# Kernel tuning notes

Measured on AMD Instinct MI355X. Metric: run time of the kernel, lower is better.

The kernel has to match this reference:

```python
import jax, jax.numpy as jnp
import numpy as np

N = 80000
E = 1280000
C_IN, HID, C_OUT = 3, 64, 1
DEPTH = 3
KS = [40000, 20000, 10000]  # ceil(0.5 * n) per pooling level
EPS = 1e-5


def gcn_conv(x, W, src, dst, ew, n, fill=2.0):
    # PyG GCNConv with add_self_loops=True; improved => self-loop weight fill=2.0
    h = x @ W                                           # [n, F]
    deg = jax.ops.segment_sum(ew, dst, num_segments=n) + fill
    dinv = jax.lax.rsqrt(deg)
    norm = dinv[src] * ew * dinv[dst]                   # [E]
    agg = jax.ops.segment_sum(norm[:, None] * h[src], dst, num_segments=n)
    return agg + (fill * dinv * dinv)[:, None] * h      # self-loop term


def batchnorm(x, gamma, beta):
    # BatchNorm1d in training mode: biased batch stats over the node dim
    mu = jnp.mean(x, axis=0)
    var = jnp.var(x, axis=0)
    return gamma * (x - mu) * jax.lax.rsqrt(var + EPS) + beta


def gcn_block(x, src, dst, ew, n, W, gamma, beta, fill=2.0):
    return jax.nn.relu(batchnorm(gcn_conv(x, W, src, dst, ew, n, fill), gamma, beta))


def topk_pool(x, src, dst, ew, w, k):
    # TopKPooling with ReLU nonlinearity: score = relu(x.w / ||w||)
    n = x.shape[0]
    score = jax.nn.relu(x @ w / jnp.linalg.norm(w))
    sc, perm = jax.lax.top_k(score, k)
    xk = x[perm] * sc[:, None]
    # filter_adj with fixed edge count: invalid edges get weight 0 (no-op in GCN)
    mapping = jnp.full((n,), -1, dtype=src.dtype).at[perm].set(
        jnp.arange(k, dtype=src.dtype))
    ns, nd = mapping[src], mapping[dst]
    valid = (ns >= 0) & (nd >= 0)
    ns = jnp.where(valid, ns, 0)
    nd = jnp.where(valid, nd, 0)
    new_ew = jnp.where(valid, ew, jnp.zeros((), ew.dtype))
    return xk, ns, nd, new_ew, perm


def _forward(x, edge_index, Wd, gd, bd, pw, Wu, gu, bu, W_out):
    src, dst = edge_index[0], edge_index[1]
    ew = jnp.ones(src.shape, x.dtype)
    n = x.shape[0]
    x = gcn_block(x, src, dst, ew, n, Wd[0], gd[0], bd[0])
    xs, sds, ews, perms = [x], [(src, dst)], [ew], []
    for i in range(DEPTH):
        x, src, dst, ew, perm = topk_pool(x, src, dst, ew, pw[i], KS[i])
        x = gcn_block(x, src, dst, ew, KS[i], Wd[i + 1], gd[i + 1], bd[i + 1])
        if i < DEPTH - 1:
            xs.append(x); sds.append((src, dst)); ews.append(ew)
        perms.append(perm)
    for i in range(DEPTH):
        j = DEPTH - 1 - i
        res = xs[j]; src, dst = sds[j]; ew = ews[j]; perm = perms[j]
        up = jnp.zeros_like(res).at[perm].set(x)
        x = res + up
        if i < DEPTH - 1:
            x = gcn_block(x, src, dst, ew, res.shape[0], Wu[i], gu[i], bu[i])
        else:
            x = jax.nn.sigmoid(
                gcn_conv(x, W_out, src, dst, ew, res.shape[0], fill=1.0))
    return x


def setup_inputs() -> dict:
    key = jax.random.key(0)
    ks = jax.random.split(key, 16)
    nrm = lambda k, shape: jax.random.normal(k, shape, jnp.float32) * 0.1
    inp = {
        "x": jax.random.normal(ks[0], (N, C_IN), jnp.float32),
        "edge_index": jax.random.randint(ks[1], (2, E), 0, N, jnp.int32),
    }
    dims = [(C_IN, HID)] + [(HID, HID)] * DEPTH
    ki = 2
    for l, (a, b) in enumerate(dims):
        inp[f"W_d{l}"] = nrm(ks[ki], (a, b)); ki += 1
        inp[f"g_d{l}"] = jnp.ones((b,), jnp.float32)
        inp[f"b_d{l}"] = jnp.zeros((b,), jnp.float32)
    for l in range(DEPTH):
        inp[f"pw{l}"] = nrm(ks[ki], (HID,)); ki += 1
    for l in range(DEPTH - 1):
        inp[f"W_u{l}"] = nrm(ks[ki], (HID, HID)); ki += 1
        inp[f"g_u{l}"] = jnp.ones((HID,), jnp.float32)
        inp[f"b_u{l}"] = jnp.zeros((HID,), jnp.float32)
    inp["W_out"] = nrm(ks[ki], (HID, C_OUT))
    return inp


def reference(x, edge_index, W_d0, g_d0, b_d0, W_d1, g_d1, b_d1, W_d2, g_d2,
              b_d2, W_d3, g_d3, b_d3, pw0, pw1, pw2, W_u0, g_u0, b_u0,
              W_u1, g_u1, b_u1, W_out):
    Wd = [W_d0, W_d1, W_d2, W_d3]
    gd = [g_d0, g_d1, g_d2, g_d3]
    bd = [b_d0, b_d1, b_d2, b_d3]
    pw = [pw0, pw1, pw2]
    Wu = [W_u0, W_u1]
    gu = [g_u0, g_u1]
    bu = [b_u0, b_u1]
    return _forward(x, edge_index, Wd, gd, bd, pw, Wu, gu, bu, W_out)
```

## Files before the change

kernel.cpp:

```cpp
#include <hip/hip_runtime.h>
#include <cstdint>
#include <utility>

#define NN0 80000
#define NE 1280000
#define MMB_GRID 1024
#define EB 2048
#define ENB 625

static inline int cdiv(int a, int b){ return (a+b-1)/b; }

__global__ void k_matmul_bn(const float* __restrict__ x, const float* __restrict__ W,
                            float* __restrict__ h, float* __restrict__ part, int n){
  __shared__ float ls[64], lq[64];
  int f = threadIdx.x & 63;
  float sa = 0.f, sq = 0.f;
  int total = n*64, stride = gridDim.x*blockDim.x;
  for (int t = blockIdx.x*blockDim.x + threadIdx.x; t < total; t += stride){
    int i = t >> 6;
    const float* xr = x + i*64;
    const float* wc = W + f;
    float s = 0.f;
    #pragma unroll
    for (int k2 = 0; k2 < 64; k2++) s += xr[k2]*wc[k2*64];
    h[t] = s; sa += s; sq += s*s;
  }
  if (threadIdx.x < 64){ ls[threadIdx.x] = 0.f; lq[threadIdx.x] = 0.f; }
  __syncthreads();
  atomicAdd(&ls[f], sa); atomicAdd(&lq[f], sq);
  __syncthreads();
  if (threadIdx.x < 128)
    part[blockIdx.x*128 + threadIdx.x] =
      (threadIdx.x < 64) ? ls[threadIdx.x] : lq[threadIdx.x-64];
}

__global__ void k_matmul_bn3(const float* __restrict__ x, const float* __restrict__ W,
                             float* __restrict__ h, float* __restrict__ part, int n){
  __shared__ float ls[64], lq[64];
  int f = threadIdx.x & 63;
  float sa = 0.f, sq = 0.f;
  int total = n*64, stride = gridDim.x*blockDim.x;
  for (int t = blockIdx.x*blockDim.x + threadIdx.x; t < total; t += stride){
    int i = t >> 6;
    float s = x[i*3]*W[f] + x[i*3+1]*W[64+f] + x[i*3+2]*W[128+f];
    h[t] = s; sa += s; sq += s*s;
  }
  if (threadIdx.x < 64){ ls[threadIdx.x] = 0.f; lq[threadIdx.x] = 0.f; }
  __syncthreads();
  atomicAdd(&ls[f], sa); atomicAdd(&lq[f], sq);
  __syncthreads();
  if (threadIdx.x < 128)
    part[blockIdx.x*128 + threadIdx.x] =
      (threadIdx.x < 64) ? ls[threadIdx.x] : lq[threadIdx.x-64];
}

__global__ void k_stats_reduce(const float* __restrict__ part, float* __restrict__ stats){
  int c = blockIdx.x, lane = threadIdx.x;
  float s = 0.f;
  for (int b = lane; b < MMB_GRID; b += 64) s += part[b*128 + c];
  for (int o = 32; o > 0; o >>= 1) s += __shfl_xor(s, o);
  if (lane == 0) stats[c] = s;
}

__global__ void k_matvec(const float* __restrict__ x, const float* __restrict__ W,
                         float* __restrict__ h1, int n){
  int lane = threadIdx.x & 63, w = threadIdx.x >> 6;
  int wid = blockIdx.x*4 + w, nw = gridDim.x*4;
  float wv = W[lane];
  for (int i = wid; i < n; i += nw){
    float v = x[i*64+lane]*wv;
    for (int o = 32; o > 0; o >>= 1) v += __shfl_xor(v, o);
    if (lane == 0) h1[i] = v;
  }
}

__global__ void k_ehist6(const int* __restrict__ key, int* __restrict__ hist, int shift){
  __shared__ int lh[64];
  if (threadIdx.x < 64) lh[threadIdx.x] = 0;
  __syncthreads();
  int base = blockIdx.x*EB + threadIdx.x;
  #pragma unroll
  for (int u = 0; u < 8; u++)
    atomicAdd(&lh[(key[base + u*256] >> shift) & 63], 1);
  __syncthreads();
  if (threadIdx.x < 64) hist[threadIdx.x*ENB + blockIdx.x] = lh[threadIdx.x];
}

__global__ void k_escatter6(const int* __restrict__ keyin, const int* __restrict__ valin,
                            int* __restrict__ keyout, int* __restrict__ valout,
                            const int* __restrict__ hist, int shift){
  __shared__ int dbase[64], run[64], wcnt[4][64];
  int t = threadIdx.x, lane = t & 63, w = t >> 6;
  if (t < 64){ dbase[t] = hist[t*ENB + blockIdx.x]; run[t] = 0; }
  __syncthreads();
  for (int u = 0; u < 8; u++){
    if (t < 64){ wcnt[0][t]=0; wcnt[1][t]=0; wcnt[2][t]=0; wcnt[3][t]=0; }
    __syncthreads();
    int g = blockIdx.x*EB + u*256 + t;
    int kk = keyin[g], vv = valin[g];
    int d = (kk >> shift) & 63;
    unsigned long long m = ~0ull;
    #pragma unroll
    for (int b = 0; b < 6; b++){
      unsigned long long bal = __ballot((d >> b) & 1);
      m &= ((d >> b) & 1) ? bal : ~bal;
    }
    int rnk = __popcll(m & ((1ull << lane) - 1ull));
    if (rnk == 0) wcnt[w][d] = __popcll(m);
    __syncthreads();
    int off2 = run[d] + rnk;
    for (int w2 = 0; w2 < w; w2++) off2 += wcnt[w2][d];
    int pos = dbase[d] + off2;
    keyout[pos] = kk; valout[pos] = vv;
    __syncthreads();
    if (t < 64) run[t] += wcnt[0][t] + wcnt[1][t] + wcnt[2][t] + wcnt[3][t];
    __syncthreads();
  }
}

__global__ void k_rp_search(const int* __restrict__ skey, int* __restrict__ rp,
                            float* __restrict__ dinvA, float* __restrict__ dinvB, int n){
  int i = blockIdx.x*blockDim.x + threadIdx.x;
  if (i >= n) return;
  int lo = 0, hi = NE;
  while (lo < hi){ int mid = (lo+hi)>>1; if (skey[mid] < i) lo = mid+1; else hi = mid; }
  int a = lo;
  lo = a; hi = NE;
  while (lo < hi){ int mid = (lo+hi)>>1; if (skey[mid] < i+1) lo = mid+1; else hi = mid; }
  int b2 = lo;
  rp[i] = a;
  if (i == n-1) rp[n] = NE;
  float deg = (float)(b2 - a);
  dinvA[i] = 1.0f/sqrtf(deg + 2.f);
  dinvB[i] = 1.0f/sqrtf(deg + 1.f);
}

__global__ void k_scan_part(const int* __restrict__ in, int* __restrict__ bsum, int n){
  __shared__ int ws[256];
  int base = blockIdx.x*1024 + threadIdx.x*4;
  int s = 0;
  #pragma unroll
  for (int u = 0; u < 4; u++){ int i = base+u; if (i < n) s += in[i]; }
  ws[threadIdx.x] = s; __syncthreads();
  for (int st = 128; st > 0; st >>= 1){
    if (threadIdx.x < st) ws[threadIdx.x] += ws[threadIdx.x+st];
    __syncthreads();
  }
  if (threadIdx.x == 0) bsum[blockIdx.x] = ws[0];
}

__global__ void k_scan_fin_rp(const int* __restrict__ in, const int* __restrict__ bsum, int nb,
                              int* __restrict__ rp, float* __restrict__ dinvA, int n){
  __shared__ int bws[256]; __shared__ int ws[256];
  int t = threadIdx.x;
  bws[t] = (t < nb) ? bsum[t] : 0; __syncthreads();
  for (int st = 1; st < 256; st <<= 1){
    int a = (t >= st) ? bws[t-st] : 0; __syncthreads();
    bws[t] += a; __syncthreads();
  }
  int blockoff = (blockIdx.x == 0) ? 0 : bws[blockIdx.x-1];
  int base = blockIdx.x*1024 + t*4;
  int v[4]; int s = 0;
  #pragma unroll
  for (int u = 0; u < 4; u++){ int i = base+u; v[u] = (i < n) ? in[i] : 0; s += v[u]; }
  ws[t] = s; __syncthreads();
  for (int st = 1; st < 256; st <<= 1){
    int a = (t >= st) ? ws[t-st] : 0; __syncthreads();
    ws[t] += a; __syncthreads();
  }
  int off = blockoff + ws[t] - s;
  #pragma unroll
  for (int u = 0; u < 4; u++){
    int i = base+u;
    if (i < n){
      rp[i] = off; off += v[u];
      dinvA[i] = 1.0f/sqrtf((float)v[u] + 2.f);
      if (i == n-1) rp[n] = off;
    }
  }
}

__global__ void k_scan_fin_flat(int* __restrict__ data, const int* __restrict__ bsum, int nb, int n){
  __shared__ int bws[256]; __shared__ int ws[256];
  int t = threadIdx.x;
  bws[t] = (t < nb) ? bsum[t] : 0; __syncthreads();
  for (int st = 1; st < 256; st <<= 1){
    int a = (t >= st) ? bws[t-st] : 0; __syncthreads();
    bws[t] += a; __syncthreads();
  }
  int blockoff = (blockIdx.x == 0) ? 0 : bws[blockIdx.x-1];
  int base = blockIdx.x*1024 + t*4;
  int v[4]; int s = 0;
  #pragma unroll
  for (int u = 0; u < 4; u++){ int i = base+u; v[u] = (i < n) ? data[i] : 0; s += v[u]; }
  ws[t] = s; __syncthreads();
  for (int st = 1; st < 256; st <<= 1){
    int a = (t >= st) ? ws[t-st] : 0; __syncthreads();
    ws[t] += a; __syncthreads();
  }
  int off = blockoff + ws[t] - s;
  #pragma unroll
  for (int u = 0; u < 4; u++){
    int i = base+u;
    if (i < n){ data[i] = off; off += v[u]; }
  }
}

__global__ void k_hist_mapped(const int* __restrict__ rp_p, const int* __restrict__ col_p,
                              const int* __restrict__ mapv, int* __restrict__ indeg, int np){
  int d = blockIdx.x*blockDim.x + threadIdx.x;
  if (d >= np) return;
  int md = mapv[d];
  if (md < 0) return;
  int c = 0, e = rp_p[d+1];
  for (int j = rp_p[d]; j < e; j++) if (mapv[col_p[j]] >= 0) c++;
  indeg[md] = c;
}
__global__ void k_scatter_mapped(const int* __restrict__ rp_p, const int* __restrict__ col_p,
                                 const int* __restrict__ mapv, const int* __restrict__ rp_c,
                                 int* __restrict__ col_c, int np){
  int d = blockIdx.x*blockDim.x + threadIdx.x;
  if (d >= np) return;
  int md = mapv[d];
  if (md < 0) return;
  int pos = rp_c[md], e = rp_p[d+1];
  for (int j = rp_p[d]; j < e; j++){
    int ms = mapv[col_p[j]];
    if (ms >= 0) col_c[pos++] = ms;
  }
}

__global__ void k_gather64(const int* __restrict__ rp, const int* __restrict__ col,
                           const float* __restrict__ dinv, const float* __restrict__ x,
                           float* __restrict__ y, int n){
  int t = blockIdx.x*blockDim.x + threadIdx.x;
  int i = t >> 6, f = t & 63;
  if (i >= n) return;
  int beg = rp[i], end = rp[i+1];
  float di = dinv[i];
  float acc = 0.f;
  for (int j = beg; j < end; j++){
    int s = col[j];
    acc += dinv[s]*x[s*64+f];
  }
  y[i*64+f] = di*acc + 2.f*di*di*x[i*64+f];
}

__global__ void k_gather3(const int* __restrict__ rp, const int* __restrict__ col,
                          const float* __restrict__ dinv, const float* __restrict__ x,
                          float* __restrict__ y, int n){
  int i = blockIdx.x*blockDim.x + threadIdx.x;
  if (i >= n) return;
  int beg = rp[i], end = rp[i+1];
  float di = dinv[i];
  float a0 = 0.f, a1 = 0.f, a2 = 0.f;
  for (int j = beg; j < end; j++){
    int s = col[j];
    float ds = dinv[s];
    a0 += ds*x[s*3+0]; a1 += ds*x[s*3+1]; a2 += ds*x[s*3+2];
  }
  float sl = 2.f*di*di;
  y[i*3+0] = di*a0 + sl*x[i*3+0];
  y[i*3+1] = di*a1 + sl*x[i*3+1];
  y[i*3+2] = di*a2 + sl*x[i*3+2];
}

__global__ void k_gather_sig(const int* __restrict__ rp, const int* __restrict__ col,
                             const float* __restrict__ dinv, const float* __restrict__ h1,
                             float* __restrict__ out, int n){
  int i = blockIdx.x*blockDim.x + threadIdx.x;
  if (i >= n) return;
  int beg = rp[i], end = rp[i+1];
  float di = dinv[i];
  float acc = 0.f;
  for (int j = beg; j < end; j++) acc += dinv[col[j]]*h1[col[j]];
  float v = di*acc + di*di*h1[i];
  out[i] = 1.f/(1.f+expf(-v));
}

__global__ void k_bnrelu(float* __restrict__ x, const float* __restrict__ stats,
                         const float* __restrict__ gamma, const float* __restrict__ beta,
                         int n) {
  int t = blockIdx.x*blockDim.x + threadIdx.x;
  if (t >= n*64) return;
  int f = t & 63;
  float inv_n = 1.0f/(float)n;
  float mu = stats[f]*inv_n;
  float var = stats[64+f]*inv_n - mu*mu;
  float v = gamma[f]*(x[t]-mu)*(1.0f/sqrtf(var+1e-5f)) + beta[f];
  x[t] = fmaxf(v, 0.f);
}

__global__ void k_bnrelu_score(float* __restrict__ x, const float* __restrict__ stats,
                               const float* __restrict__ gamma, const float* __restrict__ beta,
                               const float* __restrict__ pw,
                               float* __restrict__ score, unsigned* __restrict__ key,
                               int* __restrict__ idx, int n, int P){
  int lane = threadIdx.x & 63, w = threadIdx.x >> 6;
  int wid = blockIdx.x*4 + w, nw = gridDim.x*4;
  float inv_n = 1.f/(float)n;
  float mu = stats[lane]*inv_n;
  float var = stats[64+lane]*inv_n - mu*mu;
  float gs = gamma[lane]*(1.f/sqrtf(var+1e-5f));
  float bt = beta[lane];
  float pv = pw[lane];
  float q = pv*pv;
  for (int o = 32; o > 0; o >>= 1) q += __shfl_xor(q, o);
  float qn = 1.f/sqrtf(q);
  for (int i = wid; i < n; i += nw){
    float v = fmaxf(gs*(x[i*64+lane]-mu)+bt, 0.f);
    x[i*64+lane] = v;
    float s = v*pv;
    for (int o = 32; o > 0; o >>= 1) s += __shfl_xor(s, o);
    if (lane == 0){
      float sc = fmaxf(s*qn, 0.f);
      score[i] = sc; key[i] = ~__float_as_uint(sc); idx[i] = i;
    }
  }
  for (int g = n + wid; g < P; g += nw)
    if (lane == 0){ key[g] = 0xFFFFFFFFu; idx[g] = 0; }
}

__global__ void k_radix_hist(const unsigned* __restrict__ key, int* __restrict__ hist,
                             int shift, int nblk){
  __shared__ int lh[256];
  lh[threadIdx.x] = 0; __syncthreads();
  int base = blockIdx.x*1024 + threadIdx.x;
  #pragma unroll
  for (int u = 0; u < 4; u++){
    unsigned d = (key[base + u*256] >> shift) & 255u;
    atomicAdd(&lh[d], 1);
  }
  __syncthreads();
  hist[threadIdx.x*nblk + blockIdx.x] = lh[threadIdx.x];
}

__global__ void k_radix_scatter(const unsigned* __restrict__ keyin, const int* __restrict__ idxin,
                                unsigned* __restrict__ keyout, int* __restrict__ idxout,
                                const int* __restrict__ hist, int shift, int nblk){
  __shared__ int dbase[256], run[256], sc[256];
  __shared__ int wcnt[4][256];
  int t = threadIdx.x, lane = t & 63, w = t >> 6;
  int pre = 0, tot = 0;
  for (int b = 0; b < nblk; b++){
    int v = hist[t*nblk + b];
    if (b < blockIdx.x) pre += v;
    tot += v;
  }
  sc[t] = tot; __syncthreads();
  for (int st = 1; st < 256; st <<= 1){
    int a = (t >= st) ? sc[t-st] : 0; __syncthreads();
    sc[t] += a; __syncthreads();
  }
  dbase[t] = sc[t] - tot + pre;
  run[t] = 0;
  for (int u = 0; u < 4; u++){
    wcnt[0][t] = 0; wcnt[1][t] = 0; wcnt[2][t] = 0; wcnt[3][t] = 0;
    __syncthreads();
    int g = blockIdx.x*1024 + u*256 + t;
    unsigned kk = keyin[g]; int id = idxin[g];
    unsigned d = (kk >> shift) & 255u;
    unsigned long long m = ~0ull;
    #pragma unroll
    for (int b = 0; b < 8; b++){
      unsigned long long bal = __ballot((d >> b) & 1u);
      m &= ((d >> b) & 1u) ? bal : ~bal;
    }
    int rnk = __popcll(m & ((1ull << lane) - 1ull));
    if (rnk == 0) wcnt[w][d] = __popcll(m);
    __syncthreads();
    int off2 = run[d] + rnk;
    for (int w2 = 0; w2 < w; w2++) off2 += wcnt[w2][d];
    int pos = dbase[d] + off2;
    keyout[pos] = kk; idxout[pos] = id;
    __syncthreads();
    run[t] += wcnt[0][t] + wcnt[1][t] + wcnt[2][t] + wcnt[3][t];
    __syncthreads();
  }
}

__global__ void k_select_gather(const int* __restrict__ idxs, const float* __restrict__ x,
                                const float* __restrict__ score, int* __restrict__ perm,
                                int* __restrict__ mapv, float* __restrict__ xk, int n, int k){
  int t = blockIdx.x*blockDim.x + threadIdx.x;
  if (t < n){
    int i = idxs[t];
    mapv[i] = (t < k) ? t : -1;
    if (t < k) perm[t] = i;
  }
  if (t < k*64){
    int r = t >> 6, f = t & 63;
    int i = idxs[r];
    xk[t] = x[i*64+f]*score[i];
  }
}

__global__ void k_scatter_add(const float* __restrict__ xup, const int* __restrict__ perm,
                              float* __restrict__ res, int k) {
  int t = blockIdx.x*blockDim.x + threadIdx.x;
  if (t >= k*64) return;
  int r = t >> 6, f = t & 63;
  res[perm[r]*64+f] += xup[t];
}

extern "C" void kernel_launch(void* const* d_in, const int* in_sizes, int n_in,
                              void* d_out, int out_size, void* d_ws, size_t ws_size,
                              hipStream_t stream) {
  const float* x_in = (const float*)d_in[0];
  const int* ei = (const int*)d_in[1];
  const int* src0 = ei;
  const int* dst0 = ei + NE;
  const float* W_d[4] = {(const float*)d_in[2],(const float*)d_in[5],(const float*)d_in[8],(const float*)d_in[11]};
  const float* g_d[4] = {(const float*)d_in[3],(const float*)d_in[6],(const float*)d_in[9],(const float*)d_in[12]};
  const float* b_d[4] = {(const float*)d_in[4],(const float*)d_in[7],(const float*)d_in[10],(const float*)d_in[13]};
  const float* pw[3]  = {(const float*)d_in[14],(const float*)d_in[15],(const float*)d_in[16]};
  const float* W_u[2] = {(const float*)d_in[17],(const float*)d_in[20]};
  const float* g_u[2] = {(const float*)d_in[18],(const float*)d_in[21]};
  const float* b_u[2] = {(const float*)d_in[19],(const float*)d_in[22]};
  const float* W_out  = (const float*)d_in[23];
  float* out = (float*)d_out;

  float* base = (float*)d_ws;
  size_t off = 0;
  auto alloc = [&](size_t nf){ float* p = base + off; off += nf; return p; };
  float* x0 = alloc(5120000);
  float* x1 = alloc(2560000);
  float* x2 = alloc(1280000);
  float* x3 = alloc(640000);
  float* A  = alloc(2560000);
  float* h  = alloc(5120000);
  int* col0 = (int*)alloc(NE);
  int* col1 = (int*)alloc(NE);
  int* col2 = (int*)alloc(NE);
  int* col3 = (int*)alloc(NE);
  int* ek1 = (int*)alloc(NE);
  int* ev1 = (int*)alloc(NE);
  int* ek2 = (int*)alloc(NE);
  int* ev2 = (int*)alloc(NE);
  int* rp0 = (int*)alloc(80001);
  int* rp1 = (int*)alloc(40001);
  int* rp2 = (int*)alloc(20001);
  int* rp3 = (int*)alloc(10001);
  int* indeg  = (int*)alloc(NN0);
  float* dinv0  = alloc(NN0);
  float* dinv0f = alloc(NN0);
  float* dinv1  = alloc(40000);
  float* dinv2  = alloc(20000);
  float* dinv3  = alloc(10000);
  float* score = alloc(NN0);
  int* mapv = (int*)alloc(NN0);
  int* p0 = (int*)alloc(40000);
  int* p1 = (int*)alloc(20000);
  int* p2 = (int*)alloc(10000);
  float* stats = alloc(128);
  float* part  = alloc(MMB_GRID*128);
  unsigned* keyA = (unsigned*)alloc(81920);
  unsigned* keyB = (unsigned*)alloc(81920);
  int* idxA = (int*)alloc(81920);
  int* idxB = (int*)alloc(81920);
  int* hist = (int*)alloc(81920);
  int* ehist = (int*)alloc(64*ENB);
  int* bsum = (int*)alloc(256);
  (void)ws_size; (void)in_sizes; (void)n_in; (void)out_size;

  const int B = 256;

  auto scan_flat = [&](int* data, int n2){
    int nb = cdiv(n2, 1024);
    k_scan_part    <<<nb, 256, 0, stream>>>(data, bsum, n2);
    k_scan_fin_flat<<<nb, 256, 0, stream>>>(data, bsum, nb, n2);
  };
  auto scan_csr = [&](const int* indeg_, int* rp, float* dv, int n2){
    int nb = cdiv(n2, 1024);
    k_scan_part  <<<nb, 256, 0, stream>>>(indeg_, bsum, n2);
    k_scan_fin_rp<<<nb, 256, 0, stream>>>(indeg_, bsum, nb, rp, dv, n2);
  };

  auto conv = [&](const float* xin, int Fin, const float* W, int n,
                  const int* rp, const int* col, const float* dv, float* dstb){
    if (Fin == 3){
      k_gather3   <<<cdiv(n,B), B, 0, stream>>>(rp, col, dv, xin, h, n);
      k_matmul_bn3<<<MMB_GRID, B, 0, stream>>>(h, W, dstb, part, n);
    } else {
      k_gather64  <<<cdiv(n*64,B), B, 0, stream>>>(rp, col, dv, xin, h, n);
      k_matmul_bn <<<MMB_GRID, B, 0, stream>>>(h, W, dstb, part, n);
    }
    k_stats_reduce<<<128, 64, 0, stream>>>(part, stats);
  };

  auto pool = [&](float* xb, const float* g, const float* bt, const float* w,
                  int n, int k, int* pm, float* xk){
    int nblk = cdiv(n, 1024), P = nblk*1024;
    k_bnrelu_score<<<512, B, 0, stream>>>(xb, stats, g, bt, w, score, keyA, idxA, n, P);
    unsigned* ka = keyA; int* ia = idxA; unsigned* kb = keyB; int* ib = idxB;
    for (int pass = 0; pass < 4; pass++){
      k_radix_hist   <<<nblk, 256, 0, stream>>>(ka, hist, pass*8, nblk);
      k_radix_scatter<<<nblk, 256, 0, stream>>>(ka, ia, kb, ib, hist, pass*8, nblk);
      std::swap(ka, kb); std::swap(ia, ib);
    }
    k_select_gather<<<cdiv(k*64,B), B, 0, stream>>>(ia, xb, score, pm, mapv, xk, n, k);
  };

  auto csr_mapped = [&](const int* rp_p, const int* col_p, int np, int nc,
                        int* rp_c, int* col_c, float* dv){
    k_hist_mapped<<<cdiv(np,B), B, 0, stream>>>(rp_p, col_p, mapv, indeg, np);
    scan_csr(indeg, rp_c, dv, nc);
    k_scatter_mapped<<<cdiv(np,B), B, 0, stream>>>(rp_p, col_p, mapv, rp_c, col_c, np);
  };

  k_ehist6   <<<ENB, B, 0, stream>>>(dst0, ehist, 0);
  scan_flat(ehist, 64*ENB);
  k_escatter6<<<ENB, B, 0, stream>>>(dst0, src0, ek1, ev1, ehist, 0);
  k_ehist6   <<<ENB, B, 0, stream>>>(ek1, ehist, 6);
  scan_flat(ehist, 64*ENB);
  k_escatter6<<<ENB, B, 0, stream>>>(ek1, ev1, ek2, ev2, ehist, 6);
  k_ehist6   <<<ENB, B, 0, stream>>>(ek2, ehist, 12);
  scan_flat(ehist, 64*ENB);
  k_escatter6<<<ENB, B, 0, stream>>>(ek2, ev2, ek1, col0, ehist, 12);
  k_rp_search<<<cdiv(NN0,B), B, 0, stream>>>(ek1, rp0, dinv0, dinv0f, NN0);

  conv(x_in, 3, W_d[0], NN0, rp0, col0, dinv0, x0);
  pool(x0, g_d[0], b_d[0], pw[0], NN0, 40000, p0, A);
  csr_mapped(rp0, col0, NN0, 40000, rp1, col1, dinv1);

  conv(A, 64, W_d[1], 40000, rp1, col1, dinv1, x1);
  pool(x1, g_d[1], b_d[1], pw[1], 40000, 20000, p1, A);
  csr_mapped(rp1, col1, 40000, 20000, rp2, col2, dinv2);

  conv(A, 64, W_d[2], 20000, rp2, col2, dinv2, x2);
  pool(x2, g_d[2], b_d[2], pw[2], 20000, 10000, p2, A);
  csr_mapped(rp2, col2, 20000, 10000, rp3, col3, dinv3);

  conv(A, 64, W_d[3], 10000, rp3, col3, dinv3, x3);
  k_bnrelu<<<cdiv(10000*64,B), B, 0, stream>>>(x3, stats, g_d[3], b_d[3], 10000);

  k_scatter_add<<<cdiv(10000*64,B), B, 0, stream>>>(x3, p2, x2, 10000);
  conv(x2, 64, W_u[0], 20000, rp2, col2, dinv2, A);
  k_bnrelu<<<cdiv(20000*64,B), B, 0, stream>>>(A, stats, g_u[0], b_u[0], 20000);

  k_scatter_add<<<cdiv(20000*64,B), B, 0, stream>>>(A, p1, x1, 20000);
  conv(x1, 64, W_u[1], 40000, rp1, col1, dinv1, A);
  k_bnrelu<<<cdiv(40000*64,B), B, 0, stream>>>(A, stats, g_u[1], b_u[1], 40000);

  k_scatter_add<<<cdiv(40000*64,B), B, 0, stream>>>(A, p0, x0, 40000);

  float* h1 = score;
  k_matvec<<<512, B, 0, stream>>>(x0, W_out, h1, NN0);
  k_gather_sig<<<cdiv(NN0,B), B, 0, stream>>>(rp0, col0, dinv0f, h1, out, NN0);
}
```

Measured before the change: 809.0 us.

## Fuse 64-wide gather with matmul+BN stats and use 2-pass 9-bit edge radix sort

The CSR gather for 64-feature convs is merged with the dense matmul and batch-stat partials into one wave-per-node kernel, which removes the intermediate h buffer write and re-read. The edge sort by destination switches from three 6-bit radix passes to two 9-bit passes, cutting one histogram/scan/scatter round at the cost of larger per-block shared histograms and a larger scan. Scan blocks now process 2048 elements each. The fused conv runs the matmul from LDS per node and has less thread parallelism than the old elementwise gather kernel.

```diff
diff --git a/kernel.cpp b/kernel.cpp
--- a/kernel.cpp
+++ b/kernel.cpp
@@ -7,27 +7,39 @@
 #define MMB_GRID 1024
 #define EB 2048
 #define ENB 625
+#define E9B 512
 
 static inline int cdiv(int a, int b){ return (a+b-1)/b; }
 
-__global__ void k_matmul_bn(const float* __restrict__ x, const float* __restrict__ W,
-                            float* __restrict__ h, float* __restrict__ part, int n){
+__global__ void k_conv64(const int* __restrict__ rp, const int* __restrict__ col,
+                         const float* __restrict__ dinv, const float* __restrict__ x,
+                         const float* __restrict__ W, float* __restrict__ out,
+                         float* __restrict__ part, int n){
+  __shared__ float yl[4][64];
   __shared__ float ls[64], lq[64];
-  int f = threadIdx.x & 63;
+  int lane = threadIdx.x & 63, w = threadIdx.x >> 6;
+  if (threadIdx.x < 64){ ls[threadIdx.x] = 0.f; lq[threadIdx.x] = 0.f; }
+  __syncthreads();
   float sa = 0.f, sq = 0.f;
-  int total = n*64, stride = gridDim.x*blockDim.x;
-  for (int t = blockIdx.x*blockDim.x + threadIdx.x; t < total; t += stride){
-    int i = t >> 6;
-    const float* xr = x + i*64;
-    const float* wc = W + f;
-    float s = 0.f;
+  int wid = blockIdx.x*4 + w, nw = gridDim.x*4;
+  for (int i = wid; i < n; i += nw){
+    int beg = rp[i], end = rp[i+1];
+    float di = dinv[i];
+    float y = 0.f;
+    for (int j = beg; j < end; j++){
+      int s = col[j];
+      y += dinv[s]*x[s*64+lane];
+    }
+    y = di*y + 2.f*di*di*x[i*64+lane];
+    yl[w][lane] = y;
+    float acc = 0.f;
     #pragma unroll
-    for (int k2 = 0; k2 < 64; k2++) s += xr[k2]*wc[k2*64];
-    h[t] = s; sa += s; sq += s*s;
-  }
-  if (threadIdx.x < 64){ ls[threadIdx.x] = 0.f; lq[threadIdx.x] = 0.f; }
-  __syncthreads();
-  atomicAdd(&ls[f], sa); atomicAdd(&lq[f], sq);
+    for (int k2 = 0; k2 < 64; k2++)
+      acc += yl[w][k2]*W[k2*64+lane];
+    out[i*64+lane] = acc;
+    sa += acc; sq += acc*acc;
+  }
+  atomicAdd(&ls[lane], sa); atomicAdd(&lq[lane], sq);
   __syncthreads();
   if (threadIdx.x < 128)
     part[blockIdx.x*128 + threadIdx.x] =
@@ -74,34 +86,35 @@
   }
 }
 
-__global__ void k_ehist6(const int* __restrict__ key, int* __restrict__ hist, int shift){
-  __shared__ int lh[64];
-  if (threadIdx.x < 64) lh[threadIdx.x] = 0;
+__global__ void k_ehist9(const int* __restrict__ key, int* __restrict__ hist, int shift){
+  __shared__ int lh[E9B];
+  for (int d = threadIdx.x; d < E9B; d += 256) lh[d] = 0;
   __syncthreads();
   int base = blockIdx.x*EB + threadIdx.x;
   #pragma unroll
   for (int u = 0; u < 8; u++)
-    atomicAdd(&lh[(key[base + u*256] >> shift) & 63], 1);
-  __syncthreads();
-  if (threadIdx.x < 64) hist[threadIdx.x*ENB + blockIdx.x] = lh[threadIdx.x];
-}
-
-__global__ void k_escatter6(const int* __restrict__ keyin, const int* __restrict__ valin,
+    atomicAdd(&lh[(key[base + u*256] >> shift) & 511], 1);
+  __syncthreads();
+  for (int d = threadIdx.x; d < E9B; d += 256)
+    hist[d*ENB + blockIdx.x] = lh[d];
+}
+
+__global__ void k_escatter9(const int* __restrict__ keyin, const int* __restrict__ valin,
                             int* __restrict__ keyout, int* __restrict__ valout,
                             const int* __restrict__ hist, int shift){
-  __shared__ int dbase[64], run[64], wcnt[4][64];
+  __shared__ int dbase[E9B], run[E9B], wcnt[4][E9B];
   int t = threadIdx.x, lane = t & 63, w = t >> 6;
-  if (t < 64){ dbase[t] = hist[t*ENB + blockIdx.x]; run[t] = 0; }
+  for (int d = t; d < E9B; d += 256){ dbase[d] = hist[d*ENB + blockIdx.x]; run[d] = 0; }
   __syncthreads();
   for (int u = 0; u < 8; u++){
-    if (t < 64){ wcnt[0][t]=0; wcnt[1][t]=0; wcnt[2][t]=0; wcnt[3][t]=0; }
+    for (int d = t; d < E9B; d += 256){ wcnt[0][d]=0; wcnt[1][d]=0; wcnt[2][d]=0; wcnt[3][d]=0; }
     __syncthreads();
     int g = blockIdx.x*EB + u*256 + t;
     int kk = keyin[g], vv = valin[g];
-    int d = (kk >> shift) & 63;
+    int d = (kk >> shift) & 511;
     unsigned long long m = ~0ull;
     #pragma unroll
-    for (int b = 0; b < 6; b++){
+    for (int b = 0; b < 9; b++){
       unsigned long long bal = __ballot((d >> b) & 1);
       m &= ((d >> b) & 1) ? bal : ~bal;
     }
@@ -113,7 +126,8 @@
     int pos = dbase[d] + off2;
     keyout[pos] = kk; valout[pos] = vv;
     __syncthreads();
-    if (t < 64) run[t] += wcnt[0][t] + wcnt[1][t] + wcnt[2][t] + wcnt[3][t];
+    for (int d2 = t; d2 < E9B; d2 += 256)
+      run[d2] += wcnt[0][d2] + wcnt[1][d2] + wcnt[2][d2] + wcnt[3][d2];
     __syncthreads();
   }
 }
@@ -137,10 +151,10 @@
 
 __global__ void k_scan_part(const int* __restrict__ in, int* __restrict__ bsum, int n){
   __shared__ int ws[256];
-  int base = blockIdx.x*1024 + threadIdx.x*4;
+  int base = blockIdx.x*2048 + threadIdx.x*8;
   int s = 0;
   #pragma unroll
-  for (int u = 0; u < 4; u++){ int i = base+u; if (i < n) s += in[i]; }
+  for (int u = 0; u < 8; u++){ int i = base+u; if (i < n) s += in[i]; }
   ws[threadIdx.x] = s; __syncthreads();
   for (int st = 128; st > 0; st >>= 1){
     if (threadIdx.x < st) ws[threadIdx.x] += ws[threadIdx.x+st];
@@ -159,10 +173,10 @@
     bws[t] += a; __syncthreads();
   }
   int blockoff = (blockIdx.x == 0) ? 0 : bws[blockIdx.x-1];
-  int base = blockIdx.x*1024 + t*4;
-  int v[4]; int s = 0;
-  #pragma unroll
-  for (int u = 0; u < 4; u++){ int i = base+u; v[u] = (i < n) ? in[i] : 0; s += v[u]; }
+  int base = blockIdx.x*2048 + t*8;
+  int v[8]; int s = 0;
+  #pragma unroll
+  for (int u = 0; u < 8; u++){ int i = base+u; v[u] = (i < n) ? in[i] : 0; s += v[u]; }
   ws[t] = s; __syncthreads();
   for (int st = 1; st < 256; st <<= 1){
     int a = (t >= st) ? ws[t-st] : 0; __syncthreads();
@@ -170,7 +184,7 @@
   }
   int off = blockoff + ws[t] - s;
   #pragma unroll
-  for (int u = 0; u < 4; u++){
+  for (int u = 0; u < 8; u++){
     int i = base+u;
     if (i < n){
       rp[i] = off; off += v[u];
@@ -189,10 +203,10 @@
     bws[t] += a; __syncthreads();
   }
   int blockoff = (blockIdx.x == 0) ? 0 : bws[blockIdx.x-1];
-  int base = blockIdx.x*1024 + t*4;
-  int v[4]; int s = 0;
-  #pragma unroll
-  for (int u = 0; u < 4; u++){ int i = base+u; v[u] = (i < n) ? data[i] : 0; s += v[u]; }
+  int base = blockIdx.x*2048 + t*8;
+  int v[8]; int s = 0;
+  #pragma unroll
+  for (int u = 0; u < 8; u++){ int i = base+u; v[u] = (i < n) ? data[i] : 0; s += v[u]; }
   ws[t] = s; __syncthreads();
   for (int st = 1; st < 256; st <<= 1){
     int a = (t >= st) ? ws[t-st] : 0; __syncthreads();
@@ -200,7 +214,7 @@
   }
   int off = blockoff + ws[t] - s;
   #pragma unroll
-  for (int u = 0; u < 4; u++){
+  for (int u = 0; u < 8; u++){
     int i = base+u;
     if (i < n){ data[i] = off; off += v[u]; }
   }
@@ -228,22 +242,6 @@
     int ms = mapv[col_p[j]];
     if (ms >= 0) col_c[pos++] = ms;
   }
-}
-
-__global__ void k_gather64(const int* __restrict__ rp, const int* __restrict__ col,
-                           const float* __restrict__ dinv, const float* __restrict__ x,
-                           float* __restrict__ y, int n){
-  int t = blockIdx.x*blockDim.x + threadIdx.x;
-  int i = t >> 6, f = t & 63;
-  if (i >= n) return;
-  int beg = rp[i], end = rp[i+1];
-  float di = dinv[i];
-  float acc = 0.f;
-  for (int j = beg; j < end; j++){
-    int s = col[j];
-    acc += dinv[s]*x[s*64+f];
-  }
-  y[i*64+f] = di*acc + 2.f*di*di*x[i*64+f];
 }
 
 __global__ void k_gather3(const int* __restrict__ rp, const int* __restrict__ col,
@@ -428,7 +426,7 @@
   float* x2 = alloc(1280000);
   float* x3 = alloc(640000);
   float* A  = alloc(2560000);
-  float* h  = alloc(5120000);
+  float* h3 = alloc(240000);
   int* col0 = (int*)alloc(NE);
   int* col1 = (int*)alloc(NE);
   int* col2 = (int*)alloc(NE);
@@ -436,7 +434,6 @@
   int* ek1 = (int*)alloc(NE);
   int* ev1 = (int*)alloc(NE);
   int* ek2 = (int*)alloc(NE);
-  int* ev2 = (int*)alloc(NE);
   int* rp0 = (int*)alloc(80001);
   int* rp1 = (int*)alloc(40001);
   int* rp2 = (int*)alloc(20001);
@@ -459,32 +456,26 @@
   int* idxA = (int*)alloc(81920);
   int* idxB = (int*)alloc(81920);
   int* hist = (int*)alloc(81920);
-  int* ehist = (int*)alloc(64*ENB);
+  int* ehist = (int*)alloc(E9B*ENB);
   int* bsum = (int*)alloc(256);
   (void)ws_size; (void)in_sizes; (void)n_in; (void)out_size;
 
   const int B = 256;
 
   auto scan_flat = [&](int* data, int n2){
-    int nb = cdiv(n2, 1024);
+    int nb = cdiv(n2, 2048);
     k_scan_part    <<<nb, 256, 0, stream>>>(data, bsum, n2);
     k_scan_fin_flat<<<nb, 256, 0, stream>>>(data, bsum, nb, n2);
   };
   auto scan_csr = [&](const int* indeg_, int* rp, float* dv, int n2){
-    int nb = cdiv(n2, 1024);
+    int nb = cdiv(n2, 2048);
     k_scan_part  <<<nb, 256, 0, stream>>>(indeg_, bsum, n2);
     k_scan_fin_rp<<<nb, 256, 0, stream>>>(indeg_, bsum, nb, rp, dv, n2);
   };
 
-  auto conv = [&](const float* xin, int Fin, const float* W, int n,
+  auto conv = [&](const float* xin, const float* W, int n,
                   const int* rp, const int* col, const float* dv, float* dstb){
-    if (Fin == 3){
-      k_gather3   <<<cdiv(n,B), B, 0, stream>>>(rp, col, dv, xin, h, n);
-      k_matmul_bn3<<<MMB_GRID, B, 0, stream>>>(h, W, dstb, part, n);
-    } else {
-      k_gather64  <<<cdiv(n*64,B), B, 0, stream>>>(rp, col, dv, xin, h, n);
-      k_matmul_bn <<<MMB_GRID, B, 0, stream>>>(h, W, dstb, part, n);
-    }
+    k_conv64<<<MMB_GRID, B, 0, stream>>>(rp, col, dv, xin, W, dstb, part, n);
     k_stats_reduce<<<128, 64, 0, stream>>>(part, stats);
   };
 
@@ -508,38 +499,37 @@
     k_scatter_mapped<<<cdiv(np,B), B, 0, stream>>>(rp_p, col_p, mapv, rp_c, col_c, np);
   };
 
-  k_ehist6   <<<ENB, B, 0, stream>>>(dst0, ehist, 0);
-  scan_flat(ehist, 64*ENB);
-  k_escatter6<<<ENB, B, 0, stream>>>(dst0, src0, ek1, ev1, ehist, 0);
-  k_ehist6   <<<ENB, B, 0, stream>>>(ek1, ehist, 6);
-  scan_flat(ehist, 64*ENB);
-  k_escatter6<<<ENB, B, 0, stream>>>(ek1, ev1, ek2, ev2, ehist, 6);
-  k_ehist6   <<<ENB, B, 0, stream>>>(ek2, ehist, 12);
-  scan_flat(ehist, 64*ENB);
-  k_escatter6<<<ENB, B, 0, stream>>>(ek2, ev2, ek1, col0, ehist, 12);
-  k_rp_search<<<cdiv(NN0,B), B, 0, stream>>>(ek1, rp0, dinv0, dinv0f, NN0);
-
-  conv(x_in, 3, W_d[0], NN0, rp0, col0, dinv0, x0);
+  k_ehist9   <<<ENB, B, 0, stream>>>(dst0, ehist, 0);
+  scan_flat(ehist, E9B*ENB);
+  k_escatter9<<<ENB, B, 0, stream>>>(dst0, src0, ek1, ev1, ehist, 0);
+  k_ehist9   <<<ENB, B, 0, stream>>>(ek1, ehist, 9);
+  scan_flat(ehist, E9B*ENB);
+  k_escatter9<<<ENB, B, 0, stream>>>(ek1, ev1, ek2, col0, ehist, 9);
+  k_rp_search<<<cdiv(NN0,B), B, 0, stream>>>(ek2, rp0, dinv0, dinv0f, NN0);
+
+  k_gather3   <<<cdiv(NN0,B), B, 0, stream>>>(rp0, col0, dinv0, x_in, h3, NN0);
+  k_matmul_bn3<<<MMB_GRID, B, 0, stream>>>(h3, W_d[0], x0, part, NN0);
+  k_stats_reduce<<<128, 64, 0, stream>>>(part, stats);
   pool(x0, g_d[0], b_d[0], pw[0], NN0, 40000, p0, A);
   csr_mapped(rp0, col0, NN0, 40000, rp1, col1, dinv1);
 
-  conv(A, 64, W_d[1], 40000, rp1, col1, dinv1, x1);
+  conv(A, W_d[1], 40000, rp1, col1, dinv1, x1);
   pool(x1, g_d[1], b_d[1], pw[1], 40000, 20000, p1, A);
   csr_mapped(rp1, col1, 40000, 20000, rp2, col2, dinv2);
 
-  conv(A, 64, W_d[2], 20000, rp2, col2, dinv2, x2);
+  conv(A, W_d[2], 20000, rp2, col2, dinv2, x2);
   pool(x2, g_d[2], b_d[2], pw[2], 20000, 10000, p2, A);
   csr_mapped(rp2, col2, 20000, 10000, rp3, col3, dinv3);
 
-  conv(A, 64, W_d[3], 10000, rp3, col3, dinv3, x3);
+  conv(A, W_d[3], 10000, rp3, col3, dinv3, x3);
   k_bnrelu<<<cdiv(10000*64,B), B, 0, stream>>>(x3, stats, g_d[3], b_d[3], 10000);
 
   k_scatter_add<<<cdiv(10000*64,B), B, 0, stream>>>(x3, p2, x2, 10000);
-  conv(x2, 64, W_u[0], 20000, rp2, col2, dinv2, A);
+  conv(x2, W_u[0], 20000, rp2, col2, dinv2, A);
   k_bnrelu<<<cdiv(20000*64,B), B, 0, stream>>>(A, stats, g_u[0], b_u[0], 20000);
 
   k_scatter_add<<<cdiv(20000*64,B), B, 0, stream>>>(A, p1, x1, 20000);
-  conv(x1, 64, W_u[1], 40000, rp1, col1, dinv1, A);
+  conv(x1, W_u[1], 40000, rp1, col1, dinv1, A);
   k_bnrelu<<<cdiv(40000*64,B), B, 0, stream>>>(A, stats, g_u[1], b_u[1], 40000);
 
   k_scatter_add<<<cdiv(40000*64,B), B, 0, stream>>>(A, p0, x0, 40000);
```

Result: no change. 814.1 us (+0.6%).
